# Optimization experiments

Measured on AMD Instinct MI355X. Metric: run time of the kernel, lower is better.

Reference implementation:

```python
import jax, jax.numpy as jnp
import numpy as np

N, E = 50000, 800000
D_IN, H, D_OUT = 100, 128, 40
N_MID = 2  # num_layers(5) - 3
EPS = 1e-5


def setup_inputs() -> dict:
    key = jax.random.key(0)
    ks = iter(jax.random.split(key, 40))
    rn = lambda shape, s=0.05: jax.random.normal(next(ks), shape, dtype=jnp.float32) * s
    inp = {
        "x": jax.random.normal(next(ks), (N, D_IN), dtype=jnp.float32),
        "edge_index": jax.random.randint(next(ks), (2, E), 0, N, dtype=jnp.int64),
        "percent": 70,
        "ricci_curvature": jax.random.normal(next(ks), (E,), dtype=jnp.float32),
        # GCNConv weights/biases
        "W1": rn((D_IN, H)), "b1": jnp.zeros((H,), jnp.float32),
        "W2": rn((D_IN + H, H)), "b2": jnp.zeros((H,), jnp.float32),
        "Wm": rn((N_MID, 2 * H, H)), "bm": jnp.zeros((N_MID, H), jnp.float32),
        "Wo": rn((2 * H, D_OUT)), "bo": jnp.zeros((D_OUT,), jnp.float32),
    }
    # BatchNorm1d params + running stats (eval mode)
    def bn_params(dim, lead=()):
        return (jnp.ones(lead + (dim,), jnp.float32),            # gamma
                jnp.zeros(lead + (dim,), jnp.float32),           # beta
                rn(lead + (dim,), 0.1),                          # running mean
                1.0 + 0.1 * jax.random.uniform(next(ks), lead + (dim,), dtype=jnp.float32))  # running var
    inp["bn1_g"], inp["bn1_b"], inp["bn1_m"], inp["bn1_v"] = bn_params(D_IN)
    inp["bn2_g"], inp["bn2_b"], inp["bn2_m"], inp["bn2_v"] = bn_params(D_IN + H)
    inp["bnm_g"], inp["bnm_b"], inp["bnm_m"], inp["bnm_v"] = bn_params(2 * H, (N_MID,))
    inp["bno_g"], inp["bno_b"], inp["bno_m"], inp["bno_v"] = bn_params(2 * H)
    return inp


def reference(x, edge_index, percent, ricci_curvature,
              W1, b1, W2, b2, Wm, bm, Wo, bo,
              bn1_g, bn1_b, bn1_m, bn1_v,
              bn2_g, bn2_b, bn2_m, bn2_v,
              bnm_g, bnm_b, bnm_m, bnm_v,
              bno_g, bno_b, bno_m, bno_v):
    # Eval mode: no sampling / dynamic edge weights, dropout = identity,
    # BN uses running stats. GCNConv = PyG: add self-loops, sym-norm D^-1/2 A D^-1/2.
    n = x.shape[0]
    loop = jnp.arange(n)
    src = jnp.concatenate([edge_index[0], loop])  # [E+N]
    dst = jnp.concatenate([edge_index[1], loop])
    deg = jnp.zeros((n,), x.dtype).at[dst].add(1.0)  # >=1 thanks to self-loops
    dis = jax.lax.rsqrt(deg)
    norm = (dis[src] * dis[dst])[:, None]  # [E+N, 1]

    def gcn(h, W, b):
        hw = h @ W  # [N, out]
        agg = jnp.zeros((n, W.shape[1]), h.dtype).at[dst].add(hw[src] * norm)
        return agg + b

    def bn(h, g, bta, m, v):
        return (h - m) * (g * jax.lax.rsqrt(v + EPS)) + bta

    res = []
    x_in = x
    h = jax.nn.relu(gcn(bn(x, bn1_g, bn1_b, bn1_m, bn1_v), W1, b1))
    res.append(h)
    h = jnp.concatenate([h, x_in], axis=1)  # [N, H+D_IN]
    h = jax.nn.relu(gcn(bn(h, bn2_g, bn2_b, bn2_m, bn2_v), W2, b2))
    res.append(h)
    h = jnp.concatenate([h, res[-2]], axis=1)  # [N, 2H]
    for i in range(Wm.shape[0]):
        hi = jax.nn.relu(gcn(bn(h, bnm_g[i], bnm_b[i], bnm_m[i], bnm_v[i]), Wm[i], bm[i]))
        res.append(hi)
        h = jnp.concatenate([hi, res[-2]], axis=1)
    out = gcn(bn(h, bno_g, bno_b, bno_m, bno_v), Wo, bo)
    return (out, *res)
```

## Files before the change

kernel.cpp:

```cpp
#include <hip/hip_runtime.h>
#include <hip/hip_bf16.h>
#include <cstdint>
#include <cstddef>

#define BN_EPS 1e-5f
typedef long long ll;
using bf16x8 = __attribute__((ext_vector_type(8))) short;
using f32x4  = __attribute__((ext_vector_type(4))) float;

__device__ __forceinline__ unsigned short f2bf(float f) {
    union { float f; unsigned u; } c; c.f = f;
    unsigned u = c.u;
    u += 0x7fff + ((u >> 16) & 1);
    return (unsigned short)(u >> 16);
}
__device__ __forceinline__ float bf2f(unsigned h) {
    union { unsigned u; float f; } c; c.u = h << 16;
    return c.f;
}
__device__ __forceinline__ void addbf(float* a, uint2 v) {
    a[0] += bf2f(v.x & 0xffffu); a[1] += bf2f(v.x >> 16);
    a[2] += bf2f(v.y & 0xffffu); a[3] += bf2f(v.y >> 16);
}
__device__ __forceinline__ float4 bf4_to_f4(uint2 v) {
    return make_float4(bf2f(v.x & 0xffffu), bf2f(v.x >> 16),
                       bf2f(v.y & 0xffffu), bf2f(v.y >> 16));
}

__global__ __launch_bounds__(1024) void detect_kernel(const int* ei32, int* flag) {
    __shared__ int any;
    if (threadIdx.x == 0) any = 0;
    __syncthreads();
    for (int i = threadIdx.x; i < 2048; i += 1024) {
        if (ei32[2 * i + 1] != 0) any = 1;
    }
    __syncthreads();
    if (threadIdx.x == 0) *flag = (any == 0) ? 1 : 0;
}

__global__ void init_kernel(int* deg, int* cursor, int N) {
    int i = blockIdx.x * 256 + threadIdx.x;
    if (i < N) { deg[i] = 1; cursor[i] = 0; }
}

__global__ void count_kernel(const void* ei, int E, int* deg, const int* flag) {
    int e = blockIdx.x * 256 + threadIdx.x;
    if (e >= E) return;
    int d = (*flag) ? (int)((const ll*)ei)[(size_t)E + e]
                    : ((const int*)ei)[(size_t)E + e];
    atomicAdd(&deg[d], 1);
}

__global__ __launch_bounds__(1024) void scanA_kernel(const int* deg, int* row_ptr,
                                                     int* bsum, float* dis, int N) {
    __shared__ int wsum[16];
    int i = blockIdx.x * 1024 + threadIdx.x;
    int lane = threadIdx.x & 63, wid = threadIdx.x >> 6;
    int dv = (i < N) ? deg[i] : 1;
    if (i < N) dis[i] = rsqrtf((float)dv);
    int v = (i < N) ? (dv - 1) : 0;
    int s = v;
#pragma unroll
    for (int o = 1; o < 64; o <<= 1) { int t = __shfl_up(s, o); if (lane >= o) s += t; }
    if (lane == 63) wsum[wid] = s;
    __syncthreads();
    if (threadIdx.x < 16) {
        int w = wsum[threadIdx.x];
        int ws_ = w;
#pragma unroll
        for (int o = 1; o < 16; o <<= 1) { int t = __shfl_up(ws_, o); if ((int)threadIdx.x >= o) ws_ += t; }
        wsum[threadIdx.x] = ws_ - w;
    }
    __syncthreads();
    s += wsum[wid];
    if (i < N) row_ptr[i + 1] = s;
    if (threadIdx.x == 1023) bsum[blockIdx.x] = s;
}

__global__ void scanB_kernel(int* bsum, int nb) {
    int lane = threadIdx.x;
    int v = (lane < nb) ? bsum[lane] : 0;
    int s = v;
#pragma unroll
    for (int o = 1; o < 64; o <<= 1) { int t = __shfl_up(s, o); if (lane >= o) s += t; }
    if (lane < nb) bsum[lane] = s - v;
}

__global__ __launch_bounds__(1024) void scanC_kernel(int* row_ptr, const int* bsum, int N) {
    int i = blockIdx.x * 1024 + threadIdx.x;
    if (i < N) row_ptr[i + 1] += bsum[blockIdx.x];
    if (i == 0) row_ptr[0] = 0;
}

__global__ void fill_kernel(const void* ei, int E, const int* row_ptr,
                            int* cursor, int* csr, const int* flag) {
    int e = blockIdx.x * 256 + threadIdx.x;
    if (e >= E) return;
    int s, d;
    if (*flag) { const ll* p = (const ll*)ei; s = (int)p[e]; d = (int)p[(size_t)E + e]; }
    else       { const int* p = (const int*)ei; s = p[e]; d = p[(size_t)E + e]; }
    int pos = atomicAdd(&cursor[d], 1);
    csr[row_ptr[d] + pos] = s;
}

struct LayerP {
    const float *W, *g, *b, *m, *v;
    int K, Dout, ncb, boff;
};
struct LayerPs { LayerP l[5]; };

__global__ __launch_bounds__(256) void fold_b_all(LayerPs P,
                                                  unsigned short* __restrict__ Bhi,
                                                  unsigned short* __restrict__ Blo) {
    const LayerP& L = P.l[blockIdx.y];
    int nkc = (L.K + 31) >> 5;
    int total = nkc * L.ncb * 512;
    int idx = blockIdx.x * 256 + threadIdx.x;
    if (idx >= total) return;
    int i = idx & 7;
    int lane = (idx >> 3) & 63;
    int cb = (idx >> 9) % L.ncb;
    int kc = (idx >> 9) / L.ncb;
    int k = kc * 32 + (lane >> 4) * 8 + i;
    int col = cb * 16 + (lane & 15);
    float val = 0.f;
    if (k < L.K && col < L.Dout) {
        float s = L.g[k] * rsqrtf(L.v[k] + BN_EPS);
        val = L.W[k * L.Dout + col] * s;
    }
    unsigned short h = f2bf(val);
    Bhi[L.boff + idx] = h;
    Blo[L.boff + idx] = f2bf(val - bf2f(h));
}

__global__ __launch_bounds__(256) void fold_c_all(LayerPs P, float* __restrict__ cvecA) {
    const LayerP& L = P.l[blockIdx.y];
    int wid = threadIdx.x >> 6, lane = threadIdx.x & 63;
    int col = blockIdx.x * 4 + wid;
    float acc = 0.f;
    if (col < L.Dout) {
        for (int k = lane; k < L.K; k += 64) {
            float s = L.g[k] * rsqrtf(L.v[k] + BN_EPS);
            acc += (L.b[k] - L.m[k] * s) * L.W[k * L.Dout + col];
        }
    }
#pragma unroll
    for (int o = 32; o >= 1; o >>= 1) acc += __shfl_xor(acc, o);
    if (lane == 0 && col < 128) cvecA[128 * blockIdx.y + col] = (col < L.Dout) ? acc : 0.f;
}

template <int NCB, bool B1, bool B2>
__global__ __launch_bounds__(256) void gemm_mix_kernel(
    const void* __restrict__ X1, int K1, int ld1,
    const void* __restrict__ X2, int ld2,
    const unsigned short* __restrict__ Bhi, const unsigned short* __restrict__ Blo,
    const float* __restrict__ cvec, const float* __restrict__ dis,
    unsigned short* __restrict__ outp, int ldH, int Dout, int K, int kc_lo, int N)
{
    __shared__ float Xs[128 * 32];
    const int tid = threadIdx.x;
    const int w = tid >> 6, lane = tid & 63;
    const int lr = lane & 15, lg = lane >> 4;
    const int brow = blockIdx.x * 128;
    const int nkc = (K + 31) >> 5;

    f32x4 acc[2][NCB];
#pragma unroll
    for (int cb = 0; cb < NCB; ++cb) {
        float cv = cvec[cb * 16 + lr];
        f32x4 iv = {cv, cv, cv, cv};
        acc[0][cb] = iv;
        acc[1][cb] = iv;
    }

    for (int kc = 0; kc < nkc; ++kc) {
        const int k0 = kc * 32;
        const bool need_lo = (kc >= kc_lo);
#pragma unroll
        for (int p = 0; p < 4; ++p) {
            int fidx = (p * 256 + tid) * 4;
            int r = fidx >> 5;
            int c = fidx & 31;
            int grow = brow + r;
            int k = k0 + c;
            float4 val = make_float4(0.f, 0.f, 0.f, 0.f);
            if (grow < N) {
                if (k < K1) {
                    if (B1) val = bf4_to_f4(*(const uint2*)((const unsigned short*)X1 + (size_t)grow * ld1 + k));
                    else    val = *(const float4*)((const float*)X1 + (size_t)grow * ld1 + k);
                } else if (k < K) {
                    int kk = k - K1;
                    if (B2) val = bf4_to_f4(*(const uint2*)((const unsigned short*)X2 + (size_t)grow * ld2 + kk));
                    else    val = *(const float4*)((const float*)X2 + (size_t)grow * ld2 + kk);
                }
            }
            *(float4*)((char*)Xs + r * 128 + ((c * 4) ^ ((r & 7) << 4))) = val;
        }
        __syncthreads();

        bf16x8 ahi[2], alo[2];
#pragma unroll
        for (int rb = 0; rb < 2; ++rb) {
            int r = w * 32 + rb * 16 + lr;
            const char* base = (const char*)Xs + r * 128;
            int swz = (r & 7) << 4;
            int cb0 = lg * 32;
            float4 v0 = *(const float4*)(base + (cb0 ^ swz));
            float4 v1 = *(const float4*)(base + ((cb0 + 16) ^ swz));
            float xv[8] = {v0.x, v0.y, v0.z, v0.w, v1.x, v1.y, v1.z, v1.w};
#pragma unroll
            for (int i = 0; i < 8; ++i) {
                unsigned short h = f2bf(xv[i]);
                ahi[rb][i] = (short)h;
                alo[rb][i] = need_lo ? (short)f2bf(xv[i] - bf2f(h)) : (short)0;
            }
        }

        const bf16x8* bh = (const bf16x8*)Bhi + (size_t)kc * NCB * 64;
        const bf16x8* bl = (const bf16x8*)Blo + (size_t)kc * NCB * 64;
#pragma unroll
        for (int cb = 0; cb < NCB; ++cb) {
            bf16x8 bhf = bh[cb * 64 + lane];
            bf16x8 blf = bl[cb * 64 + lane];
#pragma unroll
            for (int rb = 0; rb < 2; ++rb) {
                acc[rb][cb] = __builtin_amdgcn_mfma_f32_16x16x32_bf16(ahi[rb], bhf, acc[rb][cb], 0, 0, 0);
                acc[rb][cb] = __builtin_amdgcn_mfma_f32_16x16x32_bf16(ahi[rb], blf, acc[rb][cb], 0, 0, 0);
                if (need_lo)
                    acc[rb][cb] = __builtin_amdgcn_mfma_f32_16x16x32_bf16(alo[rb], bhf, acc[rb][cb], 0, 0, 0);
            }
        }
        __syncthreads();
    }

#pragma unroll
    for (int rb = 0; rb < 2; ++rb) {
#pragma unroll
        for (int r = 0; r < 4; ++r) {
            int grow = brow + w * 32 + rb * 16 + lg * 4 + r;
            if (grow >= N) continue;
            float d = dis[grow];
#pragma unroll
            for (int cb = 0; cb < NCB; ++cb) {
                int col = cb * 16 + lr;
                if (col < Dout) outp[(size_t)grow * ldH + col] = f2bf(d * acc[rb][cb][r]);
            }
        }
    }
}

template <int NCB>
__global__ __launch_bounds__(256) void gemm_bf_kernel(
    const unsigned short* __restrict__ X1, int K1, int ld1,
    const unsigned short* __restrict__ X2, int ld2,
    const unsigned short* __restrict__ Bhi, const unsigned short* __restrict__ Blo,
    const float* __restrict__ cvec, const float* __restrict__ dis,
    unsigned short* __restrict__ outp, int ldH, int Dout, int K, int N)
{
    __shared__ unsigned short Xs[128 * 32];
    const int tid = threadIdx.x;
    const int w = tid >> 6, lane = tid & 63;
    const int lr = lane & 15, lg = lane >> 4;
    const int brow = blockIdx.x * 128;
    const int nkc = (K + 31) >> 5;

    f32x4 acc[2][NCB];
#pragma unroll
    for (int cb = 0; cb < NCB; ++cb) {
        float cv = cvec[cb * 16 + lr];
        f32x4 iv = {cv, cv, cv, cv};
        acc[0][cb] = iv;
        acc[1][cb] = iv;
    }

    for (int kc = 0; kc < nkc; ++kc) {
        const int k0 = kc * 32;
#pragma unroll
        for (int p = 0; p < 2; ++p) {
            int idx8 = p * 256 + tid;
            int r = idx8 >> 2;
            int cq = idx8 & 3;
            int grow = brow + r;
            int k = k0 + cq * 8;
            uint4 raw = make_uint4(0, 0, 0, 0);
            if (grow < N) {
                if (k < K1)      raw = *(const uint4*)(X1 + (size_t)grow * ld1 + k);
                else if (k < K)  raw = *(const uint4*)(X2 + (size_t)grow * ld2 + (k - K1));
            }
            *(uint4*)((char*)Xs + r * 64 + ((cq * 16) ^ ((r & 3) << 4))) = raw;
        }
        __syncthreads();

        bf16x8 ahi[2];
#pragma unroll
        for (int rb = 0; rb < 2; ++rb) {
            int r = w * 32 + rb * 16 + lr;
            ahi[rb] = *(const bf16x8*)((const char*)Xs + r * 64 + ((lg * 16) ^ ((r & 3) << 4)));
        }

        const bf16x8* bh = (const bf16x8*)Bhi + (size_t)kc * NCB * 64;
        const bf16x8* bl = (const bf16x8*)Blo + (size_t)kc * NCB * 64;
#pragma unroll
        for (int cb = 0; cb < NCB; ++cb) {
            bf16x8 bhf = bh[cb * 64 + lane];
            bf16x8 blf = bl[cb * 64 + lane];
#pragma unroll
            for (int rb = 0; rb < 2; ++rb) {
                acc[rb][cb] = __builtin_amdgcn_mfma_f32_16x16x32_bf16(ahi[rb], bhf, acc[rb][cb], 0, 0, 0);
                acc[rb][cb] = __builtin_amdgcn_mfma_f32_16x16x32_bf16(ahi[rb], blf, acc[rb][cb], 0, 0, 0);
            }
        }
        __syncthreads();
    }

#pragma unroll
    for (int rb = 0; rb < 2; ++rb) {
#pragma unroll
        for (int r = 0; r < 4; ++r) {
            int grow = brow + w * 32 + rb * 16 + lg * 4 + r;
            if (grow >= N) continue;
            float d = dis[grow];
#pragma unroll
            for (int cb = 0; cb < NCB; ++cb) {
                int col = cb * 16 + lr;
                if (col < Dout) outp[(size_t)grow * ldH + col] = f2bf(d * acc[rb][cb][r]);
            }
        }
    }
}

template <bool RELU>
__global__ __launch_bounds__(256) void agg128b_kernel(
    const unsigned short* __restrict__ hwb,
    const int* __restrict__ row_ptr, const int* __restrict__ csr,
    const float* __restrict__ dis, const float* __restrict__ bias,
    float* __restrict__ outp, unsigned short* __restrict__ hbout, int N)
{
    int wid = threadIdx.x >> 6, lane = threadIdx.x & 63;
    int node = blockIdx.x * 4 + wid;
    if (node >= N) return;
    const int half = lane >> 5, q = lane & 31;
    const uint2* hw2 = (const uint2*)hwb;
    float a[4] = {0.f, 0.f, 0.f, 0.f};
    float b4[4] = {0.f, 0.f, 0.f, 0.f};
    if (half == 0) addbf(a, hw2[(size_t)node * 32 + q]);
    int beg = row_ptr[node], end = row_ptr[node + 1];
    for (int base = beg; base < end; base += 64) {
        int idx = base + lane;
        int j = (idx < end) ? csr[idx] : 0;
        int cnt = end - base; if (cnt > 64) cnt = 64;
        int fullp = cnt >> 1;
        int t = 0;
        for (; t + 4 <= fullp; t += 4) {
            int ja = __shfl(j, 2 * t     + half);
            int jb = __shfl(j, 2 * t + 2 + half);
            int jc = __shfl(j, 2 * t + 4 + half);
            int jd = __shfl(j, 2 * t + 6 + half);
            uint2 va = hw2[(size_t)ja * 32 + q];
            uint2 vb = hw2[(size_t)jb * 32 + q];
            uint2 vc = hw2[(size_t)jc * 32 + q];
            uint2 vd = hw2[(size_t)jd * 32 + q];
            addbf(a, va); addbf(b4, vb); addbf(a, vc); addbf(b4, vd);
        }
        for (; t < fullp; ++t) {
            int ja = __shfl(j, 2 * t + half);
            uint2 va = hw2[(size_t)ja * 32 + q];
            addbf(a, va);
        }
        if (cnt & 1) {
            int ja = __shfl(j, cnt - 1);
            if (half == 0) { uint2 va = hw2[(size_t)ja * 32 + q]; addbf(a, va); }
        }
    }
#pragma unroll
    for (int c = 0; c < 4; ++c) {
        a[c] += b4[c];
        a[c] += __shfl_xor(a[c], 32);
    }
    if (half == 0) {
        float d = dis[node];
        float4 bv = ((const float4*)bias)[q];
        float4 o;
        o.x = fmaf(d, a[0], bv.x);
        o.y = fmaf(d, a[1], bv.y);
        o.z = fmaf(d, a[2], bv.z);
        o.w = fmaf(d, a[3], bv.w);
        if (RELU) {
            o.x = fmaxf(o.x, 0.f); o.y = fmaxf(o.y, 0.f);
            o.z = fmaxf(o.z, 0.f); o.w = fmaxf(o.w, 0.f);
        }
        ((float4*)outp)[(size_t)node * 32 + q] = o;
        uint2 pk;
        pk.x = (unsigned)f2bf(o.x) | ((unsigned)f2bf(o.y) << 16);
        pk.y = (unsigned)f2bf(o.z) | ((unsigned)f2bf(o.w) << 16);
        ((uint2*)hbout)[(size_t)node * 32 + q] = pk;
    }
}

__global__ __launch_bounds__(256) void agg40b_kernel(
    const unsigned short* __restrict__ hwb,
    const int* __restrict__ row_ptr, const int* __restrict__ csr,
    const float* __restrict__ dis, const float* __restrict__ bias,
    float* __restrict__ outp, int N)
{
    int wid = threadIdx.x >> 6, lane = threadIdx.x & 63;
    int node = blockIdx.x * 4 + wid;
    if (node >= N) return;
    const int half = lane >> 5, q = lane & 31;
    const bool act = q < 20;
    const unsigned* hw20 = (const unsigned*)hwb;
    float a0 = 0.f, a1 = 0.f, b0 = 0.f, b1 = 0.f;
    if (half == 0 && act) {
        unsigned v = hw20[(size_t)node * 20 + q];
        a0 += bf2f(v & 0xffffu); a1 += bf2f(v >> 16);
    }
    int beg = row_ptr[node], end = row_ptr[node + 1];
    for (int base = beg; base < end; base += 64) {
        int idx = base + lane;
        int j = (idx < end) ? csr[idx] : 0;
        int cnt = end - base; if (cnt > 64) cnt = 64;
        int fullp = cnt >> 1;
        int t = 0;
        for (; t + 4 <= fullp; t += 4) {
            int ja = __shfl(j, 2 * t     + half);
            int jb = __shfl(j, 2 * t + 2 + half);
            int jc = __shfl(j, 2 * t + 4 + half);
            int jd = __shfl(j, 2 * t + 6 + half);
            if (act) {
                unsigned va = hw20[(size_t)ja * 20 + q];
                unsigned vb = hw20[(size_t)jb * 20 + q];
                unsigned vc = hw20[(size_t)jc * 20 + q];
                unsigned vd = hw20[(size_t)jd * 20 + q];
                a0 += bf2f(va & 0xffffu); a1 += bf2f(va >> 16);
                b0 += bf2f(vb & 0xffffu); b1 += bf2f(vb >> 16);
                a0 += bf2f(vc & 0xffffu); a1 += bf2f(vc >> 16);
                b0 += bf2f(vd & 0xffffu); b1 += bf2f(vd >> 16);
            }
        }
        for (; t < fullp; ++t) {
            int ja = __shfl(j, 2 * t + half);
            if (act) {
                unsigned va = hw20[(size_t)ja * 20 + q];
                a0 += bf2f(va & 0xffffu); a1 += bf2f(va >> 16);
            }
        }
        if (cnt & 1) {
            int ja = __shfl(j, cnt - 1);
            if (half == 0 && act) {
                unsigned va = hw20[(size_t)ja * 20 + q];
                a0 += bf2f(va & 0xffffu); a1 += bf2f(va >> 16);
            }
        }
    }
    a0 += b0; a1 += b1;
    a0 += __shfl_xor(a0, 32);
    a1 += __shfl_xor(a1, 32);
    if (half == 0 && act) {
        float d = dis[node];
        float2 o;
        o.x = fmaf(d, a0, bias[2 * q]);
        o.y = fmaf(d, a1, bias[2 * q + 1]);
        *(float2*)(outp + (size_t)node * 40 + 2 * q) = o;
    }
}

extern "C" void kernel_launch(void* const* d_in, const int* in_sizes, int n_in,
                              void* d_out, int out_size, void* d_ws, size_t ws_size,
                              hipStream_t stream) {
    const int N = in_sizes[0] / 100;
    const int E = in_sizes[1] / 2;

    const float* x   = (const float*)d_in[0];
    const void*  ei  = d_in[1];
    const float* W1  = (const float*)d_in[4];
    const float* b1  = (const float*)d_in[5];
    const float* W2  = (const float*)d_in[6];
    const float* b2  = (const float*)d_in[7];
    const float* Wm  = (const float*)d_in[8];
    const float* bm  = (const float*)d_in[9];
    const float* Wo  = (const float*)d_in[10];
    const float* bo  = (const float*)d_in[11];
    const float* bn1g = (const float*)d_in[12];
    const float* bn1b = (const float*)d_in[13];
    const float* bn1m = (const float*)d_in[14];
    const float* bn1v = (const float*)d_in[15];
    const float* bn2g = (const float*)d_in[16];
    const float* bn2b = (const float*)d_in[17];
    const float* bn2m = (const float*)d_in[18];
    const float* bn2v = (const float*)d_in[19];
    const float* bnmg = (const float*)d_in[20];
    const float* bnmb = (const float*)d_in[21];
    const float* bnmm = (const float*)d_in[22];
    const float* bnmv = (const float*)d_in[23];
    const float* bnog = (const float*)d_in[24];
    const float* bnob = (const float*)d_in[25];
    const float* bnom = (const float*)d_in[26];
    const float* bnov = (const float*)d_in[27];

    char* wsb = (char*)d_ws;
    size_t off = 0;
    auto alloc = [&](size_t elems) -> void* { void* p = wsb + off; off += elems * 4; return p; };
    int*   deg     = (int*)alloc(N);
    int*   cursor  = (int*)alloc(N);
    int*   row_ptr = (int*)alloc((size_t)N + 1);
    int*   bsum    = (int*)alloc(64);
    int*   flag    = (int*)alloc(1);
    off = (off + 15) & ~(size_t)15;
    float* dis  = (float*)alloc(N);
    int*   csr  = (int*)alloc(E);
    off = (off + 15) & ~(size_t)15;
    unsigned short* hwb = (unsigned short*)alloc((size_t)N * 64);
    unsigned short* hbA = (unsigned short*)alloc((size_t)N * 64);
    unsigned short* hbB = (unsigned short*)alloc((size_t)N * 64);
    unsigned short* hbC = (unsigned short*)alloc((size_t)N * 64);
    unsigned short* BhiA = (unsigned short*)alloc(63488);
    unsigned short* BloA = (unsigned short*)alloc(63488);
    float* cvecA = (float*)alloc(128 * 5);
    (void)ws_size; (void)n_in; (void)out_size;

    float* outF = (float*)d_out;
    float* h1 = outF + (size_t)N * 40;
    float* h2 = h1 + (size_t)N * 128;
    float* h3 = h2 + (size_t)N * 128;
    float* h4 = h3 + (size_t)N * 128;

    dim3 b256(256);

    LayerPs P;
    P.l[0] = {W1, bn1g, bn1b, bn1m, bn1v, 100, 128, 8, 0};
    P.l[1] = {W2, bn2g, bn2b, bn2m, bn2v, 228, 128, 8, 16384};
    P.l[2] = {Wm, bnmg, bnmb, bnmm, bnmv, 256, 128, 8, 49152};
    P.l[3] = {Wm + 256 * 128, bnmg + 256, bnmb + 256, bnmm + 256, bnmv + 256, 256, 128, 8, 81920};
    P.l[4] = {Wo, bnog, bnob, bnom, bnov, 256, 40, 3, 114688};
    fold_b_all<<<dim3(128, 5), b256, 0, stream>>>(P, BhiA, BloA);
    fold_c_all<<<dim3(32, 5), b256, 0, stream>>>(P, cvecA);

    detect_kernel<<<1, 1024, 0, stream>>>((const int*)ei, flag);
    init_kernel<<<dim3((N + 255) / 256), b256, 0, stream>>>(deg, cursor, N);
    count_kernel<<<dim3((E + 255) / 256), b256, 0, stream>>>(ei, E, deg, flag);
    int nb = (N + 1023) / 1024;
    scanA_kernel<<<dim3(nb), dim3(1024), 0, stream>>>(deg, row_ptr, bsum, dis, N);
    scanB_kernel<<<1, 64, 0, stream>>>(bsum, nb);
    scanC_kernel<<<dim3(nb), dim3(1024), 0, stream>>>(row_ptr, bsum, N);
    fill_kernel<<<dim3((E + 255) / 256), b256, 0, stream>>>(ei, E, row_ptr, cursor, csr, flag);

    int gemm_grid = (N + 127) / 128;
    int agg_grid  = (N + 3) / 4;

    auto agg128 = [&](const float* lb, float* dst, unsigned short* hbout) {
        agg128b_kernel<true><<<dim3(agg_grid), b256, 0, stream>>>(
            hwb, row_ptr, csr, dis, lb, dst, hbout, N);
    };

    gemm_mix_kernel<8, false, false><<<dim3(gemm_grid), b256, 0, stream>>>(
        x, 100, 100, nullptr, 0, BhiA + P.l[0].boff, BloA + P.l[0].boff,
        cvecA, dis, hwb, 128, 128, 100, 0, N);
    agg128(b1, h1, hbA);

    gemm_mix_kernel<8, true, false><<<dim3(gemm_grid), b256, 0, stream>>>(
        hbA, 128, 128, x, 100, BhiA + P.l[1].boff, BloA + P.l[1].boff,
        cvecA + 128, dis, hwb, 128, 128, 228, 4, N);
    agg128(b2, h2, hbB);

    gemm_bf_kernel<8><<<dim3(gemm_grid), b256, 0, stream>>>(
        hbB, 128, 128, hbA, 128, BhiA + P.l[2].boff, BloA + P.l[2].boff,
        cvecA + 256, dis, hwb, 128, 128, 256, N);
    agg128(bm, h3, hbC);

    gemm_bf_kernel<8><<<dim3(gemm_grid), b256, 0, stream>>>(
        hbC, 128, 128, hbB, 128, BhiA + P.l[3].boff, BloA + P.l[3].boff,
        cvecA + 384, dis, hwb, 128, 128, 256, N);
    agg128(bm + 128, h4, hbA);

    gemm_bf_kernel<3><<<dim3(gemm_grid), b256, 0, stream>>>(
        hbA, 128, 128, hbC, 128, BhiA + P.l[4].boff, BloA + P.l[4].boff,
        cvecA + 512, dis, hwb, 40, 40, 256, N);
    agg40b_kernel<<<dim3(agg_grid), b256, 0, stream>>>(hwb, row_ptr, csr, dis, bo, outF, N);
}
```

Measured before the change: 454.7 us.

## Retile GEMM kernels to 64-row blocks with 64-wide K tiles

Both MFMA GEMM kernels now process 64 rows per block (one 16-row strip per wave) instead of 128, and stage 64 K-columns per shared-memory tile, running two 32-wide MFMA k-steps per barrier pair. This halves the number of __syncthreads per K, halves accumulator registers, and doubles the grid with occupancy hints in launch_bounds, aiming at better latency hiding. The cost is that each B fragment loaded from global memory is now reused by only one row block instead of two, which raises B traffic per output. The weight-fold kernel pads K chunks to an even count so the 64-wide tiles read zeros past K.

After: 432.5 us. 4.9% less time.

```diff
diff --git a/kernel.cpp b/kernel.cpp
--- a/kernel.cpp
+++ b/kernel.cpp
@@ -113,7 +113,7 @@
                                                   unsigned short* __restrict__ Bhi,
                                                   unsigned short* __restrict__ Blo) {
     const LayerP& L = P.l[blockIdx.y];
-    int nkc = (L.K + 31) >> 5;
+    int nkc = (L.K + 63) >> 6 << 1;
     int total = nkc * L.ncb * 512;
     int idx = blockIdx.x * 256 + threadIdx.x;
     if (idx >= total) return;
@@ -150,37 +150,35 @@
 }
 
 template <int NCB, bool B1, bool B2>
-__global__ __launch_bounds__(256) void gemm_mix_kernel(
+__global__ __launch_bounds__(256, 3) void gemm_mix_kernel(
     const void* __restrict__ X1, int K1, int ld1,
     const void* __restrict__ X2, int ld2,
     const unsigned short* __restrict__ Bhi, const unsigned short* __restrict__ Blo,
     const float* __restrict__ cvec, const float* __restrict__ dis,
     unsigned short* __restrict__ outp, int ldH, int Dout, int K, int kc_lo, int N)
 {
-    __shared__ float Xs[128 * 32];
+    __shared__ float Xs[64 * 64];
     const int tid = threadIdx.x;
     const int w = tid >> 6, lane = tid & 63;
     const int lr = lane & 15, lg = lane >> 4;
-    const int brow = blockIdx.x * 128;
-    const int nkc = (K + 31) >> 5;
-
-    f32x4 acc[2][NCB];
+    const int brow = blockIdx.x * 64;
+    const int nkt = (K + 63) >> 6;
+
+    f32x4 acc[NCB];
 #pragma unroll
     for (int cb = 0; cb < NCB; ++cb) {
         float cv = cvec[cb * 16 + lr];
         f32x4 iv = {cv, cv, cv, cv};
-        acc[0][cb] = iv;
-        acc[1][cb] = iv;
-    }
-
-    for (int kc = 0; kc < nkc; ++kc) {
-        const int k0 = kc * 32;
-        const bool need_lo = (kc >= kc_lo);
+        acc[cb] = iv;
+    }
+
+    for (int kt = 0; kt < nkt; ++kt) {
+        const int k0 = kt * 64;
 #pragma unroll
         for (int p = 0; p < 4; ++p) {
             int fidx = (p * 256 + tid) * 4;
-            int r = fidx >> 5;
-            int c = fidx & 31;
+            int r = fidx >> 6;
+            int c = fidx & 63;
             int grow = brow + r;
             int k = k0 + c;
             float4 val = make_float4(0.f, 0.f, 0.f, 0.f);
@@ -194,137 +192,128 @@
                     else    val = *(const float4*)((const float*)X2 + (size_t)grow * ld2 + kk);
                 }
             }
-            *(float4*)((char*)Xs + r * 128 + ((c * 4) ^ ((r & 7) << 4))) = val;
+            *(float4*)((char*)Xs + r * 256 + ((c * 4) ^ ((r & 7) << 4))) = val;
         }
         __syncthreads();
 
-        bf16x8 ahi[2], alo[2];
-#pragma unroll
-        for (int rb = 0; rb < 2; ++rb) {
-            int r = w * 32 + rb * 16 + lr;
-            const char* base = (const char*)Xs + r * 128;
-            int swz = (r & 7) << 4;
-            int cb0 = lg * 32;
+        const int r = w * 16 + lr;
+        const char* base = (const char*)Xs + r * 256;
+        const int swz = (r & 7) << 4;
+#pragma unroll
+        for (int ks = 0; ks < 2; ++ks) {
+            const int kcg = kt * 2 + ks;
+            const bool need_lo = (kcg >= kc_lo);
+            int cb0 = ks * 128 + lg * 32;
             float4 v0 = *(const float4*)(base + (cb0 ^ swz));
             float4 v1 = *(const float4*)(base + ((cb0 + 16) ^ swz));
             float xv[8] = {v0.x, v0.y, v0.z, v0.w, v1.x, v1.y, v1.z, v1.w};
+            bf16x8 ahi, alo;
 #pragma unroll
             for (int i = 0; i < 8; ++i) {
                 unsigned short h = f2bf(xv[i]);
-                ahi[rb][i] = (short)h;
-                alo[rb][i] = need_lo ? (short)f2bf(xv[i] - bf2f(h)) : (short)0;
-            }
-        }
-
-        const bf16x8* bh = (const bf16x8*)Bhi + (size_t)kc * NCB * 64;
-        const bf16x8* bl = (const bf16x8*)Blo + (size_t)kc * NCB * 64;
+                ahi[i] = (short)h;
+                alo[i] = need_lo ? (short)f2bf(xv[i] - bf2f(h)) : (short)0;
+            }
+            const bf16x8* bh = (const bf16x8*)Bhi + (size_t)kcg * NCB * 64;
+            const bf16x8* bl = (const bf16x8*)Blo + (size_t)kcg * NCB * 64;
+#pragma unroll
+            for (int cb = 0; cb < NCB; ++cb) {
+                bf16x8 bhf = bh[cb * 64 + lane];
+                bf16x8 blf = bl[cb * 64 + lane];
+                acc[cb] = __builtin_amdgcn_mfma_f32_16x16x32_bf16(ahi, bhf, acc[cb], 0, 0, 0);
+                acc[cb] = __builtin_amdgcn_mfma_f32_16x16x32_bf16(ahi, blf, acc[cb], 0, 0, 0);
+                if (need_lo)
+                    acc[cb] = __builtin_amdgcn_mfma_f32_16x16x32_bf16(alo, bhf, acc[cb], 0, 0, 0);
+            }
+        }
+        __syncthreads();
+    }
+
+#pragma unroll
+    for (int r = 0; r < 4; ++r) {
+        int grow = brow + w * 16 + lg * 4 + r;
+        if (grow >= N) continue;
+        float d = dis[grow];
 #pragma unroll
         for (int cb = 0; cb < NCB; ++cb) {
-            bf16x8 bhf = bh[cb * 64 + lane];
-            bf16x8 blf = bl[cb * 64 + lane];
-#pragma unroll
-            for (int rb = 0; rb < 2; ++rb) {
-                acc[rb][cb] = __builtin_amdgcn_mfma_f32_16x16x32_bf16(ahi[rb], bhf, acc[rb][cb], 0, 0, 0);
-                acc[rb][cb] = __builtin_amdgcn_mfma_f32_16x16x32_bf16(ahi[rb], blf, acc[rb][cb], 0, 0, 0);
-                if (need_lo)
-                    acc[rb][cb] = __builtin_amdgcn_mfma_f32_16x16x32_bf16(alo[rb], bhf, acc[rb][cb], 0, 0, 0);
-            }
-        }
-        __syncthreads();
-    }
-
-#pragma unroll
-    for (int rb = 0; rb < 2; ++rb) {
-#pragma unroll
-        for (int r = 0; r < 4; ++r) {
-            int grow = brow + w * 32 + rb * 16 + lg * 4 + r;
-            if (grow >= N) continue;
-            float d = dis[grow];
-#pragma unroll
-            for (int cb = 0; cb < NCB; ++cb) {
-                int col = cb * 16 + lr;
-                if (col < Dout) outp[(size_t)grow * ldH + col] = f2bf(d * acc[rb][cb][r]);
-            }
+            int col = cb * 16 + lr;
+            if (col < Dout) outp[(size_t)grow * ldH + col] = f2bf(d * acc[cb][r]);
         }
     }
 }
 
 template <int NCB>
-__global__ __launch_bounds__(256) void gemm_bf_kernel(
+__global__ __launch_bounds__(256, 4) void gemm_bf_kernel(
     const unsigned short* __restrict__ X1, int K1, int ld1,
     const unsigned short* __restrict__ X2, int ld2,
     const unsigned short* __restrict__ Bhi, const unsigned short* __restrict__ Blo,
     const float* __restrict__ cvec, const float* __restrict__ dis,
     unsigned short* __restrict__ outp, int ldH, int Dout, int K, int N)
 {
-    __shared__ unsigned short Xs[128 * 32];
+    __shared__ unsigned short Xs[64 * 64];
     const int tid = threadIdx.x;
     const int w = tid >> 6, lane = tid & 63;
     const int lr = lane & 15, lg = lane >> 4;
-    const int brow = blockIdx.x * 128;
-    const int nkc = (K + 31) >> 5;
-
-    f32x4 acc[2][NCB];
+    const int brow = blockIdx.x * 64;
+    const int nkt = (K + 63) >> 6;
+
+    f32x4 acc[NCB];
 #pragma unroll
     for (int cb = 0; cb < NCB; ++cb) {
         float cv = cvec[cb * 16 + lr];
         f32x4 iv = {cv, cv, cv, cv};
-        acc[0][cb] = iv;
-        acc[1][cb] = iv;
-    }
-
-    for (int kc = 0; kc < nkc; ++kc) {
-        const int k0 = kc * 32;
+        acc[cb] = iv;
+    }
+
+    for (int kt = 0; kt < nkt; ++kt) {
+        const int k0 = kt * 64;
 #pragma unroll
         for (int p = 0; p < 2; ++p) {
-            int idx8 = p * 256 + tid;
-            int r = idx8 >> 2;
-            int cq = idx8 & 3;
+            int idx = p * 256 + tid;
+            int r = idx >> 3;
+            int sl = idx & 7;
             int grow = brow + r;
-            int k = k0 + cq * 8;
+            int k = k0 + sl * 8;
             uint4 raw = make_uint4(0, 0, 0, 0);
             if (grow < N) {
                 if (k < K1)      raw = *(const uint4*)(X1 + (size_t)grow * ld1 + k);
                 else if (k < K)  raw = *(const uint4*)(X2 + (size_t)grow * ld2 + (k - K1));
             }
-            *(uint4*)((char*)Xs + r * 64 + ((cq * 16) ^ ((r & 3) << 4))) = raw;
+            *(uint4*)((char*)Xs + r * 128 + ((sl * 16) ^ ((r & 7) << 4))) = raw;
         }
         __syncthreads();
 
-        bf16x8 ahi[2];
-#pragma unroll
-        for (int rb = 0; rb < 2; ++rb) {
-            int r = w * 32 + rb * 16 + lr;
-            ahi[rb] = *(const bf16x8*)((const char*)Xs + r * 64 + ((lg * 16) ^ ((r & 3) << 4)));
-        }
-
-        const bf16x8* bh = (const bf16x8*)Bhi + (size_t)kc * NCB * 64;
-        const bf16x8* bl = (const bf16x8*)Blo + (size_t)kc * NCB * 64;
+        const int r = w * 16 + lr;
+        const char* base = (const char*)Xs + r * 128;
+        const int swz = (r & 7) << 4;
+        bf16x8 a0 = *(const bf16x8*)(base + ((lg * 16) ^ swz));
+        bf16x8 a1 = *(const bf16x8*)(base + ((64 + lg * 16) ^ swz));
+#pragma unroll
+        for (int ks = 0; ks < 2; ++ks) {
+            const int kcg = kt * 2 + ks;
+            const bf16x8 af = ks ? a1 : a0;
+            const bf16x8* bh = (const bf16x8*)Bhi + (size_t)kcg * NCB * 64;
+            const bf16x8* bl = (const bf16x8*)Blo + (size_t)kcg * NCB * 64;
+#pragma unroll
+            for (int cb = 0; cb < NCB; ++cb) {
+                bf16x8 bhf = bh[cb * 64 + lane];
+                bf16x8 blf = bl[cb * 64 + lane];
+                acc[cb] = __builtin_amdgcn_mfma_f32_16x16x32_bf16(af, bhf, acc[cb], 0, 0, 0);
+                acc[cb] = __builtin_amdgcn_mfma_f32_16x16x32_bf16(af, blf, acc[cb], 0, 0, 0);
+            }
+        }
+        __syncthreads();
+    }
+
+#pragma unroll
+    for (int r = 0; r < 4; ++r) {
+        int grow = brow + w * 16 + lg * 4 + r;
+        if (grow >= N) continue;
+        float d = dis[grow];
 #pragma unroll
         for (int cb = 0; cb < NCB; ++cb) {
-            bf16x8 bhf = bh[cb * 64 + lane];
-            bf16x8 blf = bl[cb * 64 + lane];
-#pragma unroll
-            for (int rb = 0; rb < 2; ++rb) {
-                acc[rb][cb] = __builtin_amdgcn_mfma_f32_16x16x32_bf16(ahi[rb], bhf, acc[rb][cb], 0, 0, 0);
-                acc[rb][cb] = __builtin_amdgcn_mfma_f32_16x16x32_bf16(ahi[rb], blf, acc[rb][cb], 0, 0, 0);
-            }
-        }
-        __syncthreads();
-    }
-
-#pragma unroll
-    for (int rb = 0; rb < 2; ++rb) {
-#pragma unroll
-        for (int r = 0; r < 4; ++r) {
-            int grow = brow + w * 32 + rb * 16 + lg * 4 + r;
-            if (grow >= N) continue;
-            float d = dis[grow];
-#pragma unroll
-            for (int cb = 0; cb < NCB; ++cb) {
-                int col = cb * 16 + lr;
-                if (col < Dout) outp[(size_t)grow * ldH + col] = f2bf(d * acc[rb][cb][r]);
-            }
+            int col = cb * 16 + lr;
+            if (col < Dout) outp[(size_t)grow * ldH + col] = f2bf(d * acc[cb][r]);
         }
     }
 }
@@ -544,7 +533,7 @@
     scanC_kernel<<<dim3(nb), dim3(1024), 0, stream>>>(row_ptr, bsum, N);
     fill_kernel<<<dim3((E + 255) / 256), b256, 0, stream>>>(ei, E, row_ptr, cursor, csr, flag);
 
-    int gemm_grid = (N + 127) / 128;
+    int gemm_grid = (N + 63) / 64;
     int agg_grid  = (N + 3) / 4;
 
     auto agg128 = [&](const float* lb, float* dst, unsigned short* hbout) {
```
